# Kernel optimization log

Hardware: AMD Instinct MI355X
Metric: run time of the kernel (lower is better)

Reference implementation:

```python
import jax, jax.numpy as jnp
import numpy as np

N_NODES = 30000
NEG_SLOPE = 0.2  # PyG GATConv default leaky_relu slope


def gat_conv(x, src, dst, W, a_src, a_dst, b, num_nodes, concat):
    """One PyG-style GATConv layer (add_self_loops already applied to src/dst).
    x: [N, F_in]; W: [F_in, H*C]; a_src, a_dst: [H, C]; b: [H*C] or [C].
    """
    H, C = a_src.shape
    h = (x @ W).reshape(num_nodes, H, C)                     # [N, H, C]
    alpha_src = jnp.einsum('nhc,hc->nh', h, a_src)           # [N, H]
    alpha_dst = jnp.einsum('nhc,hc->nh', h, a_dst)           # [N, H]
    e = jax.nn.leaky_relu(alpha_src[src] + alpha_dst[dst], NEG_SLOPE)  # [E, H]
    # scatter-softmax over incoming edges of each dst node
    e_max = jax.ops.segment_max(e, dst, num_segments=num_nodes)        # [N, H]
    e_exp = jnp.exp(e - e_max[dst])                                    # [E, H]
    denom = jax.ops.segment_sum(e_exp, dst, num_segments=num_nodes)    # [N, H]
    alpha = e_exp / denom[dst]                                         # [E, H]
    msg = h[src] * alpha[:, :, None]                                   # [E, H, C]
    out = jax.ops.segment_sum(msg, dst, num_segments=num_nodes)        # [N, H, C]
    out = out.reshape(num_nodes, H * C) if concat else out.mean(axis=1)
    return out + b


def _glorot(key, shape):
    fan = sum(shape[:2]) if len(shape) > 1 else shape[0] * 2
    return jax.random.normal(key, shape, dtype=jnp.float32) * np.sqrt(2.0 / fan)


def setup_inputs() -> dict:
    key = jax.random.key(0)
    ks = jax.random.split(key, 16)
    n, f_in, heads = N_NODES, 256, 4
    x = jax.random.normal(ks[0], (n, f_in), dtype=jnp.float32)
    edge_index = jax.random.randint(ks[1], (2, 480000), 0, n, dtype=jnp.int64)
    inp = {
        'x': x, 'edge_index': edge_index,
        'W1': _glorot(ks[2], (f_in, heads * 128)),
        'a1s': _glorot(ks[3], (heads, 128)), 'a1d': _glorot(ks[4], (heads, 128)),
        'b1': jnp.zeros((heads * 128,), jnp.float32),
        'W2': _glorot(ks[5], (heads * 128, heads * 128)),
        'a2s': _glorot(ks[6], (heads, 128)), 'a2d': _glorot(ks[7], (heads, 128)),
        'b2': jnp.zeros((heads * 128,), jnp.float32),
        'W3': _glorot(ks[8], (heads * 128, heads * 64)),
        'a3s': _glorot(ks[9], (heads, 64)), 'a3d': _glorot(ks[10], (heads, 64)),
        'b3': jnp.zeros((heads * 64,), jnp.float32),
        # conv4: 256 -> 64, 1 head, mean (concat=False)
        'W4': _glorot(ks[11], (heads * 64, 64)),
        'a4s': _glorot(ks[12], (1, 64)), 'a4d': _glorot(ks[13], (1, 64)),
        'b4': jnp.zeros((64,), jnp.float32),
    }
    return inp


def reference(x, edge_index, W1, a1s, a1d, b1, W2, a2s, a2d, b2,
              W3, a3s, a3d, b3, W4, a4s, a4d, b4):
    n = x.shape[0]
    # PyG GATConv default add_self_loops=True
    loops = jnp.arange(n, dtype=edge_index.dtype)
    src = jnp.concatenate([edge_index[0], loops])
    dst = jnp.concatenate([edge_index[1], loops])
    h = jax.nn.relu(gat_conv(x, src, dst, W1, a1s, a1d, b1, n, True))
    h = jax.nn.relu(gat_conv(h, src, dst, W2, a2s, a2d, b2, n, True))
    h = jax.nn.relu(gat_conv(h, src, dst, W3, a3s, a3d, b3, n, True))
    h = jax.nn.relu(gat_conv(h, src, dst, W4, a4s, a4d, b4, n, False))
    return h
```

## Files before the change

kernel.cpp:

```cpp
#include <hip/hip_runtime.h>
#include <hip/hip_fp16.h>
#include <math.h>


typedef __attribute__((ext_vector_type(8))) _Float16 f16x8;
typedef __attribute__((ext_vector_type(4))) float floatx4;
typedef __attribute__((ext_vector_type(8))) unsigned short usv8;
typedef __attribute__((ext_vector_type(4))) unsigned short usv4;

#define DEG_CAP 256

__device__ __forceinline__ float lrelu(float e) {
    return (e > 0.f) ? e : 0.2f * e;
}
__device__ __forceinline__ void gload16(const void* g, void* l) {
    __builtin_amdgcn_global_load_lds(
        (const __attribute__((address_space(1))) void*)g,
        (__attribute__((address_space(3))) void*)l, 16, 0, 0);
}
__device__ __forceinline__ float ushort2floath(unsigned short u) {
    union { unsigned short u; __half h; } cv;
    cv.u = u;
    return __half2float(cv.h);
}

static __global__ void zero_int(int* __restrict__ p, int n) {
    int i = blockIdx.x * blockDim.x + threadIdx.x;
    if (i < n) p[i] = 0;
}

static __global__ void hist_kernel(const int* __restrict__ ei, int e0, int n_nodes,
                                   int* __restrict__ counts) {
    int e = blockIdx.x * blockDim.x + threadIdx.x;
    int et = e0 + n_nodes;
    if (e >= et) return;
    int d = (e < e0) ? ei[e0 + e] : (e - e0);
    atomicAdd(&counts[d], 1);
}

static __global__ void scan_kernel(const int* __restrict__ counts,
                                   int* __restrict__ row_ptr,
                                   int* __restrict__ cursor, int n) {
    __shared__ int sdata[1024];
    int tid = threadIdx.x;
    int per = (n + 1023) / 1024;
    int start = tid * per;
    int stop = min(start + per, n);
    if (start > n) start = n;
    int s = 0;
    for (int i = start; i < stop; i++) s += counts[i];
    sdata[tid] = s;
    __syncthreads();
    for (int off = 1; off < 1024; off <<= 1) {
        int t = (tid >= off) ? sdata[tid - off] : 0;
        __syncthreads();
        sdata[tid] += t;
        __syncthreads();
    }
    int run = sdata[tid] - s;
    for (int i = start; i < stop; i++) {
        row_ptr[i] = run;
        cursor[i] = run;
        run += counts[i];
    }
    if (stop == n) row_ptr[n] = run;
}

static __global__ void scatter_kernel(const int* __restrict__ ei, int e0, int n_nodes,
                                      int* __restrict__ cursor,
                                      int* __restrict__ src_sorted) {
    int e = blockIdx.x * blockDim.x + threadIdx.x;
    int et = e0 + n_nodes;
    if (e >= et) return;
    int s, d;
    if (e < e0) { s = ei[e]; d = ei[e0 + e]; } else { s = e - e0; d = s; }
    int pos = atomicAdd(&cursor[d], 1);
    src_sorted[pos] = s;
}

__device__ __forceinline__ void convW_one(const float* W, __half* BT,
                                          int idx, int K, int N) {
    int n = idx / K, k = idx % K;
    float v = (n < N) ? W[(size_t)k * N + n] : 0.f;
    BT[(size_t)n * K + k] = __float2half(v);
}

static __global__ void conv_all(const float* __restrict__ X, __half* __restrict__ A, int nx,
                                const float* __restrict__ W1, __half* __restrict__ BT1,
                                const float* __restrict__ W2, __half* __restrict__ BT2,
                                const float* __restrict__ W3, __half* __restrict__ BT3,
                                const float* __restrict__ W4, __half* __restrict__ BT4,
                                float* __restrict__ zero_as, int nzero) {
    int idx = blockIdx.x * 256 + threadIdx.x;
    if (idx < nx) { A[idx] = __float2half(X[idx]); return; }
    idx -= nx;
    if (idx < 131072) { convW_one(W1, BT1, idx, 256, 512); return; }
    idx -= 131072;
    if (idx < 262144) { convW_one(W2, BT2, idx, 512, 512); return; }
    idx -= 262144;
    if (idx < 131072) { convW_one(W3, BT3, idx, 512, 256); return; }
    idx -= 131072;
    if (idx < 32768)  { convW_one(W4, BT4, idx, 256, 64); return; }
    idx -= 32768;
    if (idx < nzero) zero_as[idx] = 0.f;
}

#define BM 128
#define BN 128
#define BKK 64

__launch_bounds__(256, 4)
static __global__ void gemm_mfma(const __half* __restrict__ A,
                                 const __half* __restrict__ B,
                                 __half* __restrict__ C, int M, int K, int N,
                                 int xcols, int mblocks,
                                 const float* __restrict__ asv,
                                 const float* __restrict__ adv,
                                 float* __restrict__ as_out,
                                 float* __restrict__ ad_out,
                                 int Hh, int Cc) {
    __shared__ __align__(16) __half lds[2 * BM * BKK];
    const int tid  = threadIdx.x;
    const int lane = tid & 63;
    const int wave = tid >> 6;

    const int id = blockIdx.x;
    const int band = id / (8 * xcols);
    const int rem = id - band * 8 * xcols;
    const int band_rows = min(8, mblocks - band * 8);
    const int ry = rem % band_rows;
    const int rx = rem / band_rows;
    const int r0 = (band * 8 + ry) * BM;
    const int c0 = rx * BN;

    const int wm = (wave >> 1) * 64;
    const int wn = (wave & 1) * 64;
    const int q   = lane >> 4;
    const int m16 = lane & 15;

    floatx4 acc[4][4];
#pragma unroll
    for (int i = 0; i < 4; i++)
#pragma unroll
        for (int j = 0; j < 4; j++) acc[i][j] = {0.f, 0.f, 0.f, 0.f};

    char* ldsb = (char*)lds;

#pragma unroll 1
    for (int k0 = 0; k0 < K; k0 += BKK) {
        __syncthreads();
#pragma unroll
        for (int c = 0; c < 4; c++) {
            int slot = c * 256 + tid;
            int row = slot >> 3;
            int gc  = (slot & 7) ^ (row & 7);
            gload16(A + (size_t)(r0 + row) * K + k0 + gc * 8,
                    ldsb + slot * 16);
            gload16(B + (size_t)(c0 + row) * K + k0 + gc * 8,
                    ldsb + 16384 + slot * 16);
        }
        __syncthreads();
#pragma unroll
        for (int ks = 0; ks < 2; ks++) {
            f16x8 af[4], bf[4];
#pragma unroll
            for (int i = 0; i < 4; i++) {
                int row = wm + i * 16 + m16;
                int ch  = (q + ks * 4) ^ (row & 7);
                af[i] = *(const f16x8*)(ldsb + (row * 8 + ch) * 16);
            }
#pragma unroll
            for (int j = 0; j < 4; j++) {
                int row = wn + j * 16 + m16;
                int ch  = (q + ks * 4) ^ (row & 7);
                bf[j] = *(const f16x8*)(ldsb + 16384 + (row * 8 + ch) * 16);
            }
#pragma unroll
            for (int i = 0; i < 4; i++)
#pragma unroll
                for (int j = 0; j < 4; j++)
                    acc[i][j] = __builtin_amdgcn_mfma_f32_16x16x32_f16(
                        af[i], bf[j], acc[i][j], 0, 0, 0);
        }
    }
#pragma unroll
    for (int i = 0; i < 4; i++)
#pragma unroll
        for (int j = 0; j < 4; j++)
#pragma unroll
            for (int r = 0; r < 4; r++) {
                int row = r0 + wm + i * 16 + q * 4 + r;
                int col = c0 + wn + j * 16 + m16;
                if (row < M && col < N)
                    C[(size_t)row * N + col] = __float2half(acc[i][j][r]);
            }
    if (c0 + wn < N) {
        int head = (c0 + wn) / Cc;
#pragma unroll
        for (int i = 0; i < 4; i++)
#pragma unroll
            for (int r = 0; r < 4; r++) {
                float ps = 0.f, pd = 0.f;
#pragma unroll
                for (int j = 0; j < 4; j++) {
                    int c = c0 + wn + j * 16 + m16;
                    float v = acc[i][j][r];
                    ps = fmaf(v, asv[c], ps);
                    pd = fmaf(v, adv[c], pd);
                }
#pragma unroll
                for (int off = 1; off < 16; off <<= 1) {
                    ps += __shfl_xor(ps, off);
                    pd += __shfl_xor(pd, off);
                }
                if (m16 == 0) {
                    int row = r0 + wm + i * 16 + q * 4 + r;
                    if (row < M) {
                        atomicAdd(&as_out[(size_t)row * Hh + head], ps);
                        atomicAdd(&ad_out[(size_t)row * Hh + head], pd);
                    }
                }
            }
    }
}

template <int H>
__launch_bounds__(256)
static __global__ void stats_kernel(const float* __restrict__ as_arr,
                                    const float* __restrict__ ad_arr,
                                    const int* __restrict__ row_ptr,
                                    const int* __restrict__ src_sorted,
                                    __half* __restrict__ w_arr, int Epad,
                                    float* __restrict__ znext_as,
                                    float* __restrict__ znext_ad, int n_nodes) {
    __shared__ float lds_e[4][DEG_CAP * H];
    int wave = threadIdx.x >> 6;
    int lane = threadIdx.x & 63;
    int n = blockIdx.x * 4 + wave;
    if (n >= n_nodes) return;
    int beg = row_ptr[n], end = row_ptr[n + 1];
    float* we = lds_e[wave];

    float ad_h[H], m_h[H], l_h[H];
#pragma unroll
    for (int hh = 0; hh < H; hh++) {
        ad_h[hh] = ad_arr[(size_t)n * H + hh];
        m_h[hh] = -INFINITY;
        l_h[hh] = 0.f;
    }
    for (int base = beg; base < end; base += 64) {
        int j = base + lane;
        bool ok = j < end;
        float e_h[H];
        if (ok) {
            int s = src_sorted[j];
            if constexpr (H == 4) {
                float4 a = ((const float4*)as_arr)[s];
                e_h[0] = lrelu(a.x + ad_h[0]);
                e_h[1] = lrelu(a.y + ad_h[1]);
                e_h[2] = lrelu(a.z + ad_h[2]);
                e_h[3] = lrelu(a.w + ad_h[3]);
            } else {
                e_h[0] = lrelu(as_arr[s] + ad_h[0]);
            }
            int idx = j - beg;
            if (idx < DEG_CAP) {
                if constexpr (H == 4) {
                    *(float4*)&we[idx * 4] = make_float4(e_h[0], e_h[1], e_h[2], e_h[3]);
                } else {
                    we[idx] = e_h[0];
                }
            }
        } else {
#pragma unroll
            for (int hh = 0; hh < H; hh++) e_h[hh] = -INFINITY;
        }
#pragma unroll
        for (int hh = 0; hh < H; hh++) {
            float cm = e_h[hh];
#pragma unroll
            for (int off = 1; off < 64; off <<= 1) cm = fmaxf(cm, __shfl_xor(cm, off));
            float newm = fmaxf(m_h[hh], cm);
            float p = ok ? __expf(e_h[hh] - newm) : 0.f;
#pragma unroll
            for (int off = 1; off < 64; off <<= 1) p += __shfl_xor(p, off);
            l_h[hh] = l_h[hh] * __expf(m_h[hh] - newm) + p;
            m_h[hh] = newm;
        }
    }
    float inv_h[H];
#pragma unroll
    for (int hh = 0; hh < H; hh++) inv_h[hh] = 1.f / l_h[hh];

    unsigned short* wp = (unsigned short*)w_arr;
    for (int base = beg; base < end; base += 64) {
        int j = base + lane;
        if (j < end) {
            int idx = j - beg;
            float e_h[H];
            if (idx < DEG_CAP) {
                if constexpr (H == 4) {
                    float4 t = *(float4*)&we[idx * 4];
                    e_h[0] = t.x; e_h[1] = t.y; e_h[2] = t.z; e_h[3] = t.w;
                } else {
                    e_h[0] = we[idx];
                }
            } else {
                int s = src_sorted[j];
                if constexpr (H == 4) {
                    float4 a = ((const float4*)as_arr)[s];
                    e_h[0] = lrelu(a.x + ad_h[0]);
                    e_h[1] = lrelu(a.y + ad_h[1]);
                    e_h[2] = lrelu(a.z + ad_h[2]);
                    e_h[3] = lrelu(a.w + ad_h[3]);
                } else {
                    e_h[0] = lrelu(as_arr[s] + ad_h[0]);
                }
            }
#pragma unroll
            for (int hh = 0; hh < H; hh++)
                __builtin_nontemporal_store(
                    __half_as_ushort(__float2half(
                        __expf(e_h[hh] - m_h[hh]) * inv_h[hh])),
                    wp + (size_t)hh * Epad + j);
        }
    }

    if (znext_as != nullptr && lane == 0) {
        if constexpr (H == 4) {
            *(float4*)&znext_as[(size_t)n * 4] = make_float4(0.f, 0.f, 0.f, 0.f);
            *(float4*)&znext_ad[(size_t)n * 4] = make_float4(0.f, 0.f, 0.f, 0.f);
        } else {
            znext_as[n] = 0.f;
            znext_ad[n] = 0.f;
        }
    }
}

template <int H, int C, bool F16OUT>
__launch_bounds__(256)
static __global__ void gather_slice(const __half* __restrict__ h,
                                    const __half* __restrict__ w_arr,
                                    const int* __restrict__ row_ptr,
                                    const int* __restrict__ src_sorted,
                                    const float* __restrict__ bias,
                                    float* __restrict__ outf,
                                    __half* __restrict__ outh,
                                    int n_nodes, int Epad) {
    constexpr int K = H * C;
    constexpr int NSLICE = K / 64;
    const int wave = threadIdx.x >> 6;
    const int lane = threadIdx.x & 63;
    const int g  = lane >> 3;
    const int cg = lane & 7;
    const int slice = blockIdx.x % NSLICE;
    const int group = blockIdx.x / NSLICE;
    const int colbase = slice * 64 + cg * 8;
    const int head = (slice * 64) / C;
    const unsigned short* wp = (const unsigned short*)w_arr + (size_t)head * Epad;

    float bloc[8];
    {
        float4 b0 = *(const float4*)(bias + colbase);
        float4 b1 = *(const float4*)(bias + colbase + 4);
        bloc[0] = b0.x; bloc[1] = b0.y; bloc[2] = b0.z; bloc[3] = b0.w;
        bloc[4] = b1.x; bloc[5] = b1.y; bloc[6] = b1.z; bloc[7] = b1.w;
    }

    const int n = (group * 4 + wave) * 8 + g;
    const bool valid = n < n_nodes;
    int beg = 0, end = 0;
    if (valid) { beg = row_ptr[n]; end = row_ptr[n + 1]; }

    float acc[8];
#pragma unroll
    for (int r = 0; r < 8; r++) acc[r] = 0.f;

    int j = beg;
    for (; j + 1 < end; j += 2) {
        int s0 = __builtin_nontemporal_load(src_sorted + j);
        int s1 = __builtin_nontemporal_load(src_sorted + j + 1);
        float w0 = ushort2floath(__builtin_nontemporal_load(wp + j));
        float w1 = ushort2floath(__builtin_nontemporal_load(wp + j + 1));
        float4 r0 = *(const float4*)(h + (size_t)s0 * K + colbase);
        float4 r1 = *(const float4*)(h + (size_t)s1 * K + colbase);
        const __half* h0 = (const __half*)&r0;
        const __half* h1 = (const __half*)&r1;
#pragma unroll
        for (int r = 0; r < 8; r++)
            acc[r] = fmaf(w0, __half2float(h0[r]), acc[r]);
#pragma unroll
        for (int r = 0; r < 8; r++)
            acc[r] = fmaf(w1, __half2float(h1[r]), acc[r]);
    }
    if (j < end) {
        int s0 = __builtin_nontemporal_load(src_sorted + j);
        float w0 = ushort2floath(__builtin_nontemporal_load(wp + j));
        float4 r0 = *(const float4*)(h + (size_t)s0 * K + colbase);
        const __half* h0 = (const __half*)&r0;
#pragma unroll
        for (int r = 0; r < 8; r++)
            acc[r] = fmaf(w0, __half2float(h0[r]), acc[r]);
    }

    if (valid) {
        float v[8];
#pragma unroll
        for (int r = 0; r < 8; r++) v[r] = fmaxf(acc[r] + bloc[r], 0.f);
        if constexpr (F16OUT) {
            usv8 o;
#pragma unroll
            for (int r = 0; r < 8; r++)
                o[r] = __half_as_ushort(__float2half(v[r]));
            __builtin_nontemporal_store(
                o, (usv8*)((unsigned short*)outh + (size_t)n * K + colbase));
        } else {
            floatx4 o0 = {v[0], v[1], v[2], v[3]};
            floatx4 o1 = {v[4], v[5], v[6], v[7]};
            __builtin_nontemporal_store(
                o0, (floatx4*)(outf + (size_t)n * K + colbase));
            __builtin_nontemporal_store(
                o1, (floatx4*)(outf + (size_t)n * K + colbase + 4));
        }
    }
}


static inline size_t align_up(size_t x) { return (x + 255) & ~(size_t)255; }

extern "C" void kernel_launch(void* const* d_in, const int* in_sizes, int n_in,
                              void* d_out, int out_size, void* d_ws, size_t ws_size,
                              hipStream_t stream) {
    const float* x   = (const float*)d_in[0];
    const int*   ei  = (const int*)d_in[1];
    const float* W1  = (const float*)d_in[2];
    const float* a1s = (const float*)d_in[3];
    const float* a1d = (const float*)d_in[4];
    const float* b1  = (const float*)d_in[5];
    const float* W2  = (const float*)d_in[6];
    const float* a2s = (const float*)d_in[7];
    const float* a2d = (const float*)d_in[8];
    const float* b2  = (const float*)d_in[9];
    const float* W3  = (const float*)d_in[10];
    const float* a3s = (const float*)d_in[11];
    const float* a3d = (const float*)d_in[12];
    const float* b3  = (const float*)d_in[13];
    const float* W4  = (const float*)d_in[14];
    const float* a4s = (const float*)d_in[15];
    const float* a4d = (const float*)d_in[16];
    const float* b4  = (const float*)d_in[17];

    const int n  = in_sizes[0] / 256;
    const int e0 = in_sizes[1] / 2;
    const int et = e0 + n;
    const int Mpad = ((n + 127) / 128) * 128;
    const int Epad = ((et + 255) / 256) * 256;

    char* w = (char*)d_ws;
    __half* bufA = (__half*)w;                   w += align_up((size_t)Mpad * 512 * 2);
    __half* bufB = (__half*)w;                   w += align_up((size_t)Mpad * 512 * 2);
    __half* hbuf = (__half*)w;                   w += align_up((size_t)Mpad * 512 * 2);
    __half* WT1 = (__half*)w;                    w += align_up((size_t)512 * 256 * 2);
    __half* WT2 = (__half*)w;                    w += align_up((size_t)512 * 512 * 2);
    __half* WT3 = (__half*)w;                    w += align_up((size_t)256 * 512 * 2);
    __half* WT4 = (__half*)w;                    w += align_up((size_t)128 * 256 * 2);
    float* asA = (float*)w;                      w += align_up((size_t)n * 4 * 4);
    float* adA = (float*)w;                      w += align_up((size_t)n * 4 * 4);
    float* asB = (float*)w;                      w += align_up((size_t)n * 4 * 4);
    float* adB = (float*)w;                      w += align_up((size_t)n * 4 * 4);
    int* row_ptr = (int*)w;                      w += align_up((size_t)(n + 1) * 4);
    int* counts  = (int*)w;                      w += align_up((size_t)n * 4);
    int* cursor  = (int*)w;                      w += align_up((size_t)n * 4);
    int* src_sorted = (int*)w;                   w += align_up((size_t)et * 4);
    __half* wbuf = (__half*)w;                   w += align_up((size_t)Epad * 4 * 2);
    (void)ws_size;

    dim3 blk(256);
    int nodeblocks = (n + 3) / 4;
    int ggrp = (n + 31) / 32;

    zero_int<<<(n + 255) / 256, 256, 0, stream>>>(counts, n);
    hist_kernel<<<(et + 255) / 256, 256, 0, stream>>>(ei, e0, n, counts);
    scan_kernel<<<1, 1024, 0, stream>>>(counts, row_ptr, cursor, n);
    scatter_kernel<<<(et + 255) / 256, 256, 0, stream>>>(ei, e0, n, cursor, src_sorted);

    const int nx = n * 256;
    conv_all<<<(nx + 557056 + n * 8 + 255) / 256, blk, 0, stream>>>(
        x, bufA, nx, W1, WT1, W2, WT2, W3, WT3, W4, WT4, asA, n * 8);

    const int mblocks = Mpad / 128;

    gemm_mfma<<<dim3(4 * mblocks), blk, 0, stream>>>(bufA, WT1, hbuf, n, 256, 512, 4, mblocks,
                                                     a1s, a1d, asA, adA, 4, 128);
    stats_kernel<4><<<nodeblocks, blk, 0, stream>>>(asA, adA, row_ptr, src_sorted, wbuf, Epad, asB, adB, n);
    gather_slice<4, 128, true><<<dim3(8 * ggrp), blk, 0, stream>>>(
        hbuf, wbuf, row_ptr, src_sorted, b1, nullptr, bufB, n, Epad);

    gemm_mfma<<<dim3(4 * mblocks), blk, 0, stream>>>(bufB, WT2, hbuf, n, 512, 512, 4, mblocks,
                                                     a2s, a2d, asB, adB, 4, 128);
    stats_kernel<4><<<nodeblocks, blk, 0, stream>>>(asB, adB, row_ptr, src_sorted, wbuf, Epad, asA, adA, n);
    gather_slice<4, 128, true><<<dim3(8 * ggrp), blk, 0, stream>>>(
        hbuf, wbuf, row_ptr, src_sorted, b2, nullptr, bufA, n, Epad);

    gemm_mfma<<<dim3(2 * mblocks), blk, 0, stream>>>(bufA, WT3, hbuf, n, 512, 256, 2, mblocks,
                                                     a3s, a3d, asA, adA, 4, 64);
    stats_kernel<4><<<nodeblocks, blk, 0, stream>>>(asA, adA, row_ptr, src_sorted, wbuf, Epad, asB, adB, n);
    gather_slice<4, 64, true><<<dim3(4 * ggrp), blk, 0, stream>>>(
        hbuf, wbuf, row_ptr, src_sorted, b3, nullptr, bufB, n, Epad);

    gemm_mfma<<<dim3(1 * mblocks), blk, 0, stream>>>(bufB, WT4, hbuf, n, 256, 64, 1, mblocks,
                                                     a4s, a4d, asB, adB, 1, 64);
    stats_kernel<1><<<nodeblocks, blk, 0, stream>>>(asB, adB, row_ptr, src_sorted, wbuf, Epad, nullptr, nullptr, n);
    gather_slice<1, 64, false><<<dim3(1 * ggrp), blk, 0, stream>>>(
        hbuf, wbuf, row_ptr, src_sorted, b4, (float*)d_out, nullptr, n, Epad);
}
```

Before: 680.9 us.

## Sort nodes by in-degree so gather waves process similar-degree rows

Adds a counting sort of nodes by in-degree (histogram, scan, scatter) and has gather_slice process nodes in that order. Each wave then handles 8 nodes with similar edge counts, which is meant to cut the divergence where lanes sit idle waiting for the highest-degree node. It also drops the nontemporal hints on src_sorted and weight loads. The cost is four extra small launches plus an indirection load. Output writes now follow a permuted node order, so they are scattered instead of contiguous.

```diff
diff --git a/kernel.cpp b/kernel.cpp
--- a/kernel.cpp
+++ b/kernel.cpp
@@ -9,6 +9,7 @@
 typedef __attribute__((ext_vector_type(4))) unsigned short usv4;
 
 #define DEG_CAP 256
+#define DBUCKETS 1024
 
 __device__ __forceinline__ float lrelu(float e) {
     return (e > 0.f) ? e : 0.2f * e;
@@ -76,6 +77,24 @@
     if (e < e0) { s = ei[e]; d = ei[e0 + e]; } else { s = e - e0; d = s; }
     int pos = atomicAdd(&cursor[d], 1);
     src_sorted[pos] = s;
+}
+
+static __global__ void deg_hist_kernel(const int* __restrict__ counts, int n,
+                                       int* __restrict__ dhist) {
+    int i = blockIdx.x * blockDim.x + threadIdx.x;
+    if (i >= n) return;
+    int b = min(counts[i], DBUCKETS - 1);
+    atomicAdd(&dhist[b], 1);
+}
+
+static __global__ void order_scatter_kernel(const int* __restrict__ counts, int n,
+                                            int* __restrict__ dcur,
+                                            int* __restrict__ node_order) {
+    int i = blockIdx.x * blockDim.x + threadIdx.x;
+    if (i >= n) return;
+    int b = min(counts[i], DBUCKETS - 1);
+    int pos = atomicAdd(&dcur[b], 1);
+    node_order[pos] = i;
 }
 
 __device__ __forceinline__ void convW_one(const float* W, __half* BT,
@@ -343,6 +362,7 @@
                                     const __half* __restrict__ w_arr,
                                     const int* __restrict__ row_ptr,
                                     const int* __restrict__ src_sorted,
+                                    const int* __restrict__ node_order,
                                     const float* __restrict__ bias,
                                     float* __restrict__ outf,
                                     __half* __restrict__ outh,
@@ -367,10 +387,14 @@
         bloc[4] = b1.x; bloc[5] = b1.y; bloc[6] = b1.z; bloc[7] = b1.w;
     }
 
-    const int n = (group * 4 + wave) * 8 + g;
-    const bool valid = n < n_nodes;
-    int beg = 0, end = 0;
-    if (valid) { beg = row_ptr[n]; end = row_ptr[n + 1]; }
+    const int idx = (group * 4 + wave) * 8 + g;
+    const bool valid = idx < n_nodes;
+    int n = 0, beg = 0, end = 0;
+    if (valid) {
+        n = node_order[idx];
+        beg = row_ptr[n];
+        end = row_ptr[n + 1];
+    }
 
     float acc[8];
 #pragma unroll
@@ -378,10 +402,10 @@
 
     int j = beg;
     for (; j + 1 < end; j += 2) {
-        int s0 = __builtin_nontemporal_load(src_sorted + j);
-        int s1 = __builtin_nontemporal_load(src_sorted + j + 1);
-        float w0 = ushort2floath(__builtin_nontemporal_load(wp + j));
-        float w1 = ushort2floath(__builtin_nontemporal_load(wp + j + 1));
+        int s0 = src_sorted[j];
+        int s1 = src_sorted[j + 1];
+        float w0 = ushort2floath(wp[j]);
+        float w1 = ushort2floath(wp[j + 1]);
         float4 r0 = *(const float4*)(h + (size_t)s0 * K + colbase);
         float4 r1 = *(const float4*)(h + (size_t)s1 * K + colbase);
         const __half* h0 = (const __half*)&r0;
@@ -394,8 +418,8 @@
             acc[r] = fmaf(w1, __half2float(h1[r]), acc[r]);
     }
     if (j < end) {
-        int s0 = __builtin_nontemporal_load(src_sorted + j);
-        float w0 = ushort2floath(__builtin_nontemporal_load(wp + j));
+        int s0 = src_sorted[j];
+        float w0 = ushort2floath(wp[j]);
         float4 r0 = *(const float4*)(h + (size_t)s0 * K + colbase);
         const __half* h0 = (const __half*)&r0;
 #pragma unroll
@@ -473,6 +497,10 @@
     int* cursor  = (int*)w;                      w += align_up((size_t)n * 4);
     int* src_sorted = (int*)w;                   w += align_up((size_t)et * 4);
     __half* wbuf = (__half*)w;                   w += align_up((size_t)Epad * 4 * 2);
+    int* node_order = (int*)w;                   w += align_up((size_t)n * 4);
+    int* dhist = (int*)w;                        w += align_up((size_t)DBUCKETS * 4);
+    int* drp   = (int*)w;                        w += align_up((size_t)(DBUCKETS + 1) * 4);
+    int* dcur  = (int*)w;                        w += align_up((size_t)DBUCKETS * 4);
     (void)ws_size;
 
     dim3 blk(256);
@@ -484,6 +512,11 @@
     scan_kernel<<<1, 1024, 0, stream>>>(counts, row_ptr, cursor, n);
     scatter_kernel<<<(et + 255) / 256, 256, 0, stream>>>(ei, e0, n, cursor, src_sorted);
 
+    zero_int<<<(DBUCKETS + 255) / 256, 256, 0, stream>>>(dhist, DBUCKETS);
+    deg_hist_kernel<<<(n + 255) / 256, 256, 0, stream>>>(counts, n, dhist);
+    scan_kernel<<<1, 1024, 0, stream>>>(dhist, drp, dcur, DBUCKETS);
+    order_scatter_kernel<<<(n + 255) / 256, 256, 0, stream>>>(counts, n, dcur, node_order);
+
     const int nx = n * 256;
     conv_all<<<(nx + 557056 + n * 8 + 255) / 256, blk, 0, stream>>>(
         x, bufA, nx, W1, WT1, W2, WT2, W3, WT3, W4, WT4, asA, n * 8);
@@ -494,23 +527,23 @@
                                                      a1s, a1d, asA, adA, 4, 128);
     stats_kernel<4><<<nodeblocks, blk, 0, stream>>>(asA, adA, row_ptr, src_sorted, wbuf, Epad, asB, adB, n);
     gather_slice<4, 128, true><<<dim3(8 * ggrp), blk, 0, stream>>>(
-        hbuf, wbuf, row_ptr, src_sorted, b1, nullptr, bufB, n, Epad);
+        hbuf, wbuf, row_ptr, src_sorted, node_order, b1, nullptr, bufB, n, Epad);
 
     gemm_mfma<<<dim3(4 * mblocks), blk, 0, stream>>>(bufB, WT2, hbuf, n, 512, 512, 4, mblocks,
                                                      a2s, a2d, asB, adB, 4, 128);
     stats_kernel<4><<<nodeblocks, blk, 0, stream>>>(asB, adB, row_ptr, src_sorted, wbuf, Epad, asA, adA, n);
     gather_slice<4, 128, true><<<dim3(8 * ggrp), blk, 0, stream>>>(
-        hbuf, wbuf, row_ptr, src_sorted, b2, nullptr, bufA, n, Epad);
+        hbuf, wbuf, row_ptr, src_sorted, node_order, b2, nullptr, bufA, n, Epad);
 
     gemm_mfma<<<dim3(2 * mblocks), blk, 0, stream>>>(bufA, WT3, hbuf, n, 512, 256, 2, mblocks,
                                                      a3s, a3d, asA, adA, 4, 64);
     stats_kernel<4><<<nodeblocks, blk, 0, stream>>>(asA, adA, row_ptr, src_sorted, wbuf, Epad, asB, adB, n);
     gather_slice<4, 64, true><<<dim3(4 * ggrp), blk, 0, stream>>>(
-        hbuf, wbuf, row_ptr, src_sorted, b3, nullptr, bufB, n, Epad);
+        hbuf, wbuf, row_ptr, src_sorted, node_order, b3, nullptr, bufB, n, Epad);
 
     gemm_mfma<<<dim3(1 * mblocks), blk, 0, stream>>>(bufB, WT4, hbuf, n, 256, 64, 1, mblocks,
                                                      a4s, a4d, asB, adB, 1, 64);
     stats_kernel<1><<<nodeblocks, blk, 0, stream>>>(asB, adB, row_ptr, src_sorted, wbuf, Epad, nullptr, nullptr, n);
     gather_slice<1, 64, false><<<dim3(1 * ggrp), blk, 0, stream>>>(
-        hbuf, wbuf, row_ptr, src_sorted, b4, (float*)d_out, nullptr, n, Epad);
-}
+        hbuf, wbuf, row_ptr, src_sorted, node_order, b4, (float*)d_out, nullptr, n, Epad);
+}
```

After: 780.1 us. 1.15x slower.
